# Kernel optimization log

Hardware: AMD Instinct MI355X
Metric: run time of the kernel (lower is better)

Reference implementation:

```python
import jax, jax.numpy as jnp
import numpy as np

N_NODES = 100_000
N_EDGES = 3_200_000
F_IN = 64
HID = 16
N_CLASSES = 4


def setup_inputs() -> dict:
    key = jax.random.key(0)
    ks = jax.random.split(key, 9)
    x = jax.random.normal(ks[0], (N_NODES, F_IN), dtype=jnp.float32)
    edge_index = jax.random.randint(ks[1], (2, N_EDGES), 0, N_NODES, dtype=jnp.int64)
    edge_weight = jax.random.uniform(ks[2], (N_EDGES,), dtype=jnp.float32)
    # Glorot-style init for the three GCN layer weights, zero bias (PyG default)
    W1 = jax.random.normal(ks[3], (F_IN, HID), dtype=jnp.float32) * (1.0 / np.sqrt(F_IN))
    b1 = jnp.zeros((HID,), jnp.float32)
    W3 = jax.random.normal(ks[4], (HID, HID), dtype=jnp.float32) * (1.0 / np.sqrt(HID))
    b3 = jnp.zeros((HID,), jnp.float32)
    W2 = jax.random.normal(ks[5], (HID, N_CLASSES), dtype=jnp.float32) * (1.0 / np.sqrt(HID))
    b2 = jnp.zeros((N_CLASSES,), jnp.float32)
    return {"x": x, "edge_index": edge_index, "edge_weight": edge_weight,
            "W1": W1, "b1": b1, "W3": W3, "b3": b3, "W2": W2, "b2": b2}


def reference(x, edge_index, edge_weight, W1, b1, W3, b3, W2, b2):
    n = x.shape[0]
    # GCNConv default: add self-loops with weight 1, symmetric deg^-1/2 norm
    loop = jnp.arange(n, dtype=edge_index.dtype)
    row = jnp.concatenate([edge_index[0], loop])  # source nodes
    col = jnp.concatenate([edge_index[1], loop])  # target nodes
    ew = jnp.concatenate([edge_weight, jnp.ones((n,), edge_weight.dtype)])
    deg = jax.ops.segment_sum(ew, col, num_segments=n)
    dinv = jnp.where(deg > 0, jax.lax.rsqrt(deg), 0.0)
    norm = dinv[row] * ew * dinv[col]  # [E+N]

    def gcn_conv(h, W, b):
        h = h @ W                                  # [N, out] small matmul first
        msg = norm[:, None] * h[row]               # gather + scale, [E+N, out]
        return jax.ops.segment_sum(msg, col, num_segments=n) + b

    h = jax.nn.relu(gcn_conv(x, W1, b1))
    # dropout is identity in eval mode (training=False)
    h = jax.nn.relu(gcn_conv(h, W3, b3))
    h = gcn_conv(h, W2, b2)
    return jax.nn.log_softmax(h, axis=1)
```

## Files before the change

kernel.cpp:

```cpp
#include <hip/hip_runtime.h>
#include <math.h>

#define NN 100000
#define NE 3200000
#define F_IN 64
#define HID 16
#define NC 4

#define SZB 256
#define NB 391
#define CAP 10240
#define CH 8192
#define NCH 391

typedef _Float16 half_t;
typedef _Float16 h4f __attribute__((ext_vector_type(4)));

__global__ __launch_bounds__(512) void k_initcur(int* __restrict__ cursor) {
    int i = threadIdx.x;
    if (i < NB) cursor[i] = i * CAP;
}

__global__ __launch_bounds__(1024) void k_bin(const int* __restrict__ row,
                                              const int* __restrict__ col,
                                              const float* __restrict__ ew,
                                              int* __restrict__ cursor,
                                              uint2* __restrict__ bin) {
    __shared__ int h[NB];
    __shared__ int lstart[NB + 1];
    __shared__ int gbase[NB];
    __shared__ int ps[512];
    __shared__ uint2 stage[CH];
    int tid = threadIdx.x;
    for (int i = tid; i < NB; i += 1024) h[i] = 0;
    __syncthreads();
    int e0 = blockIdx.x * CH;
    int e1 = min(e0 + CH, NE);
    int eCnt = e1 - e0;
    for (int i = e0 + tid * 4; i < e1; i += 1024 * 4) {
        int4 c4 = *(const int4*)(col + i);
        atomicAdd(&h[c4.x >> 8], 1);
        atomicAdd(&h[c4.y >> 8], 1);
        atomicAdd(&h[c4.z >> 8], 1);
        atomicAdd(&h[c4.w >> 8], 1);
    }
    __syncthreads();
    int c0 = (tid < NB) ? h[tid] : 0;
    if (tid < 512) ps[tid] = c0;
    for (int off = 1; off < 512; off <<= 1) {
        __syncthreads();
        int v = (tid < 512 && tid >= off) ? ps[tid - off] : 0;
        __syncthreads();
        if (tid < 512) ps[tid] += v;
    }
    __syncthreads();
    if (tid < NB) {
        int ex = ps[tid] - c0;
        lstart[tid] = ex;
        h[tid] = ex;
        if (c0) gbase[tid] = atomicAdd(&cursor[tid], c0);
    }
    if (tid == 0) lstart[NB] = eCnt;
    __syncthreads();
    for (int i = e0 + tid * 4; i < e1; i += 1024 * 4) {
        int4 c4 = *(const int4*)(col + i);
        int4 r4 = *(const int4*)(row + i);
        float4 w4 = *(const float4*)(ew + i);
        int p;
        p = atomicAdd(&h[c4.x >> 8], 1);
        stage[p] = make_uint2(((unsigned)r4.x << 8) | (c4.x & 255), __float_as_uint(w4.x));
        p = atomicAdd(&h[c4.y >> 8], 1);
        stage[p] = make_uint2(((unsigned)r4.y << 8) | (c4.y & 255), __float_as_uint(w4.y));
        p = atomicAdd(&h[c4.z >> 8], 1);
        stage[p] = make_uint2(((unsigned)r4.z << 8) | (c4.z & 255), __float_as_uint(w4.z));
        p = atomicAdd(&h[c4.w >> 8], 1);
        stage[p] = make_uint2(((unsigned)r4.w << 8) | (c4.w & 255), __float_as_uint(w4.w));
    }
    __syncthreads();
    for (int i = tid; i < eCnt; i += 1024) {
        int lo = 0, hi = NB;
        while (hi - lo > 1) {
            int mid = (lo + hi) >> 1;
            if (lstart[mid] <= i) lo = mid; else hi = mid;
        }
        int d = gbase[lo] + (i - lstart[lo]);
        if (d < (lo + 1) * CAP)
            bin[d] = stage[i];
    }
}

__global__ __launch_bounds__(1024) void k_sort(const uint2* __restrict__ bin,
                                               const int* __restrict__ cursor,
                                               unsigned* __restrict__ ekey,
                                               half_t* __restrict__ ew16,
                                               int2* __restrict__ nodeptr2,
                                               float* __restrict__ dinv) {
    __shared__ int cnt[SZB];
    __shared__ float wdeg[SZB];
    __shared__ int ps[SZB];
    __shared__ int curp[SZB];
    __shared__ int mpad_s;
    __shared__ unsigned skey_st[CAP];
    __shared__ half_t sw_st[CAP];
    int b = blockIdx.x, tid = threadIdx.x;
    if (tid < SZB) { cnt[tid] = 0; wdeg[tid] = 0.0f; }
    __syncthreads();
    int s = b * CAP;
    int e = min(cursor[b], s + CAP);
    for (int i = s + tid; i < e; i += 1024) {
        uint2 u = bin[i];
        int cl = u.x & 255;
        atomicAdd(&cnt[cl], 1);
        atomicAdd(&wdeg[cl], __uint_as_float(u.y));
    }
    __syncthreads();
    int pc = (tid < SZB) ? ((cnt[tid] + 3) & ~3) : 0;
    if (tid < SZB) ps[tid] = pc;
    for (int off = 1; off < SZB; off <<= 1) {
        __syncthreads();
        int v = (tid < SZB && tid >= off) ? ps[tid - off] : 0;
        __syncthreads();
        if (tid < SZB) ps[tid] += v;
    }
    __syncthreads();
    if (tid < SZB) {
        int ex = ps[tid] - pc;
        curp[tid] = ex;
        int n = b * SZB + tid;
        if (n < NN) {
            nodeptr2[n] = make_int2(s + ex, s + ex + pc);
            dinv[n] = rsqrtf(1.0f + wdeg[tid]);
        }
        if (tid == SZB - 1) mpad_s = ps[tid];
    }
    __syncthreads();
    int mpad = mpad_s;
    for (int i = tid; i < mpad; i += 1024) {
        skey_st[i] = 0u;
        sw_st[i] = (half_t)0.0f;
    }
    __syncthreads();
    for (int i = s + tid; i < e; i += 1024) {
        uint2 u = bin[i];
        int cl = u.x & 255;
        int pos = atomicAdd(&curp[cl], 1);
        skey_st[pos] = u.x >> 8;
        sw_st[pos] = (half_t)__uint_as_float(u.y);
    }
    __syncthreads();
    for (int i = tid; i < mpad; i += 1024) {
        ekey[s + i] = skey_st[i];
        ew16[s + i] = sw_st[i];
    }
}

__global__ __launch_bounds__(256) void k_xform1(const float* __restrict__ x,
                                                const float* __restrict__ W,
                                                const float* __restrict__ dinv,
                                                half_t* __restrict__ tt) {
    __shared__ float Ws[F_IN * HID];
    for (int i = threadIdx.x; i < F_IN * HID; i += 256) Ws[i] = W[i];
    __syncthreads();
    int n = blockIdx.x * blockDim.x + threadIdx.x;
    if (n >= NN) return;
    float acc[HID];
#pragma unroll
    for (int j = 0; j < HID; j++) acc[j] = 0.0f;
    const float4* xp = (const float4*)(x + (size_t)n * F_IN);
#pragma unroll
    for (int k4 = 0; k4 < F_IN / 4; k4++) {
        float4 v = xp[k4];
        int k = k4 * 4;
#pragma unroll
        for (int j = 0; j < HID; j++) {
            acc[j] += v.x * Ws[(k + 0) * HID + j];
            acc[j] += v.y * Ws[(k + 1) * HID + j];
            acc[j] += v.z * Ws[(k + 2) * HID + j];
            acc[j] += v.w * Ws[(k + 3) * HID + j];
        }
    }
    float di = dinv[n];
    h4f* op = (h4f*)(tt + (size_t)n * HID);
#pragma unroll
    for (int g = 0; g < 4; g++) {
        h4f o;
        o.x = (half_t)(di * acc[g * 4 + 0]);
        o.y = (half_t)(di * acc[g * 4 + 1]);
        o.z = (half_t)(di * acc[g * 4 + 2]);
        o.w = (half_t)(di * acc[g * 4 + 3]);
        op[g] = o;
    }
}

template <int DN>
__global__ __launch_bounds__(256) void k_aggf(const unsigned* __restrict__ ekey,
                                              const half_t* __restrict__ ew16,
                                              const int2* __restrict__ nptr,
                                              const half_t* __restrict__ tt_in,
                                              const float* __restrict__ bias,
                                              const float* __restrict__ dinv,
                                              const float* __restrict__ Wn,
                                              half_t* __restrict__ tt_out) {
    __shared__ float Ws[HID * DN];
    if (threadIdx.x < HID * DN) Ws[threadIdx.x] = Wn[threadIdx.x];
    __syncthreads();
    int tid = blockIdx.x * 256 + threadIdx.x;
    int n = tid >> 2;
    int l = tid & 3;
    if (n >= NN) return;
    int2 p = nptr[n];
    const h4f* ttp = (const h4f*)tt_in;
    h4f sv = ttp[n * 4 + l];
    float ax = 0.f, ay = 0.f, az = 0.f, aw = 0.f;
    for (int base = p.x; base < p.y; base += 4) {
        int4 k4 = *(const int4*)(ekey + base);
        h4f w4 = *(const h4f*)(ew16 + base);
        h4f v0 = ttp[k4.x * 4 + l];
        h4f v1 = ttp[k4.y * 4 + l];
        h4f v2 = ttp[k4.z * 4 + l];
        h4f v3 = ttp[k4.w * 4 + l];
        float w0 = (float)w4.x, w1 = (float)w4.y, w2 = (float)w4.z, w3 = (float)w4.w;
        ax += w0 * (float)v0.x; ay += w0 * (float)v0.y; az += w0 * (float)v0.z; aw += w0 * (float)v0.w;
        ax += w1 * (float)v1.x; ay += w1 * (float)v1.y; az += w1 * (float)v1.z; aw += w1 * (float)v1.w;
        ax += w2 * (float)v2.x; ay += w2 * (float)v2.y; az += w2 * (float)v2.z; aw += w2 * (float)v2.w;
        ax += w3 * (float)v3.x; ay += w3 * (float)v3.y; az += w3 * (float)v3.z; aw += w3 * (float)v3.w;
    }
    float di = dinv[n];
    const float4* b4p = (const float4*)bias;
    float4 b4 = b4p[l];
    float hreg[4];
    hreg[0] = fmaxf(b4.x + di * (ax + (float)sv.x), 0.f);
    hreg[1] = fmaxf(b4.y + di * (ay + (float)sv.y), 0.f);
    hreg[2] = fmaxf(b4.z + di * (az + (float)sv.z), 0.f);
    hreg[3] = fmaxf(b4.w + di * (aw + (float)sv.w), 0.f);
    if (DN == 16) {
        float ox = 0.f, oy = 0.f, oz = 0.f, ow = 0.f;
#pragma unroll
        for (int k = 0; k < HID; k++) {
            float hk = __shfl(hreg[k & 3], k >> 2, 4);
            const float4 wk = *(const float4*)&Ws[k * 16 + 4 * l];
            ox += hk * wk.x; oy += hk * wk.y; oz += hk * wk.z; ow += hk * wk.w;
        }
        h4f ov;
        ov.x = (half_t)(di * ox); ov.y = (half_t)(di * oy);
        ov.z = (half_t)(di * oz); ov.w = (half_t)(di * ow);
        ((h4f*)tt_out)[n * 4 + l] = ov;
    } else {
        float o = 0.f;
#pragma unroll
        for (int k = 0; k < HID; k++) {
            float hk = __shfl(hreg[k & 3], k >> 2, 4);
            o += hk * Ws[k * DN + l];
        }
        tt_out[(size_t)n * DN + l] = (half_t)(di * o);
    }
}

__global__ __launch_bounds__(256) void k_agg4sm(const unsigned* __restrict__ ekey,
                                                const half_t* __restrict__ ew16,
                                                const int2* __restrict__ nptr,
                                                const half_t* __restrict__ tt,
                                                const float* __restrict__ bias,
                                                const float* __restrict__ dinv,
                                                float* __restrict__ out) {
    int tid = blockIdx.x * 256 + threadIdx.x;
    int n = tid >> 2;
    int l = tid & 3;
    if (n >= NN) return;
    int2 p = nptr[n];
    float self = (float)tt[n * 4 + l];
    float acc = 0.f;
    for (int base = p.x; base < p.y; base += 4) {
        int4 k4 = *(const int4*)(ekey + base);
        h4f w4 = *(const h4f*)(ew16 + base);
        acc += (float)w4.x * (float)tt[k4.x * 4 + l];
        acc += (float)w4.y * (float)tt[k4.y * 4 + l];
        acc += (float)w4.z * (float)tt[k4.z * 4 + l];
        acc += (float)w4.w * (float)tt[k4.w * 4 + l];
    }
    float di = dinv[n];
    float logit = bias[l] + di * (acc + self);
    float m = logit;
    m = fmaxf(m, __shfl_xor(m, 1, 4));
    m = fmaxf(m, __shfl_xor(m, 2, 4));
    float ex = expf(logit - m);
    float s = ex;
    s += __shfl_xor(s, 1, 4);
    s += __shfl_xor(s, 2, 4);
    out[n * 4 + l] = logit - m - logf(s);
}

extern "C" void kernel_launch(void* const* d_in, const int* in_sizes, int n_in,
                              void* d_out, int out_size, void* d_ws, size_t ws_size,
                              hipStream_t stream) {
    const float* x  = (const float*)d_in[0];
    const int*   ei = (const int*)d_in[1];
    const float* ew = (const float*)d_in[2];
    const float* W1 = (const float*)d_in[3];
    const float* b1 = (const float*)d_in[4];
    const float* W3 = (const float*)d_in[5];
    const float* b3 = (const float*)d_in[6];
    const float* W2 = (const float*)d_in[7];
    const float* b2 = (const float*)d_in[8];
    float* out = (float*)d_out;

    const int* row = ei;
    const int* col = ei + NE;

    const size_t NEP = (size_t)NB * CAP;
    char* ws = (char*)d_ws;
    size_t off = 0;
    float*    dinv     = (float*)(ws + off);    off += 400000;
    int2*     nodeptr2 = (int2*)(ws + off);     off += 800000;
    int*      cursor   = (int*)(ws + off);      off += 2048;
    unsigned* ekey     = (unsigned*)(ws + off); off += NEP * 4;
    half_t*   ew16     = (half_t*)(ws + off);   off += NEP * 2;
    uint2*    bin      = (uint2*)(ws + off);    off += NEP * 8;
    half_t*   tt1      = (half_t*)(ws + off);   off += (size_t)NN * HID * 2;
    half_t*   tt2      = (half_t*)(ws + off);   off += (size_t)NN * HID * 2;
    half_t*   tt3      = (half_t*)(ws + off);   off += (size_t)NN * NC * 2;

    k_initcur<<<1, 512, 0, stream>>>(cursor);
    k_bin<<<NCH, 1024, 0, stream>>>(row, col, ew, cursor, bin);
    k_sort<<<NB, 1024, 0, stream>>>(bin, cursor, ekey, ew16, nodeptr2, dinv);

    int gN = (NN + 255) / 256;
    int gA = (NN * 4 + 255) / 256;

    k_xform1<<<gN, 256, 0, stream>>>(x, W1, dinv, tt1);
    k_aggf<HID><<<gA, 256, 0, stream>>>(ekey, ew16, nodeptr2, tt1, b1, dinv, W3, tt2);
    k_aggf<NC><<<gA, 256, 0, stream>>>(ekey, ew16, nodeptr2, tt2, b3, dinv, W2, tt3);
    k_agg4sm<<<gA, 256, 0, stream>>>(ekey, ew16, nodeptr2, tt3, b2, dinv, out);
}
```

Baseline: 255.1 us.

## Pack edge key and fp16 weight into one word; fuse first transform into sort

New measurement: 249.9 us. 1.02x faster.

```diff
diff --git a/kernel.cpp b/kernel.cpp
--- a/kernel.cpp
+++ b/kernel.cpp
@@ -16,9 +16,11 @@
 typedef _Float16 half_t;
 typedef _Float16 h4f __attribute__((ext_vector_type(4)));
 
-__global__ __launch_bounds__(512) void k_initcur(int* __restrict__ cursor) {
-    int i = threadIdx.x;
-    if (i < NB) cursor[i] = i * CAP;
+__device__ __forceinline__ float upw(int pk) {
+    unsigned short us = (unsigned short)(pk & 0x7fff);
+    half_t h;
+    __builtin_memcpy(&h, &us, 2);
+    return (float)h;
 }
 
 __global__ __launch_bounds__(1024) void k_bin(const int* __restrict__ row,
@@ -58,7 +60,7 @@
         int ex = ps[tid] - c0;
         lstart[tid] = ex;
         h[tid] = ex;
-        if (c0) gbase[tid] = atomicAdd(&cursor[tid], c0);
+        if (c0) gbase[tid] = tid * CAP + atomicAdd(&cursor[tid], c0);
     }
     if (tid == 0) lstart[NB] = eCnt;
     __syncthreads();
@@ -91,22 +93,26 @@
 
 __global__ __launch_bounds__(1024) void k_sort(const uint2* __restrict__ bin,
                                                const int* __restrict__ cursor,
-                                               unsigned* __restrict__ ekey,
-                                               half_t* __restrict__ ew16,
+                                               const float* __restrict__ x,
+                                               const float* __restrict__ W1,
+                                               unsigned* __restrict__ epk,
                                                int2* __restrict__ nodeptr2,
-                                               float* __restrict__ dinv) {
+                                               float* __restrict__ dinv,
+                                               half_t* __restrict__ tt1) {
     __shared__ int cnt[SZB];
     __shared__ float wdeg[SZB];
     __shared__ int ps[SZB];
     __shared__ int curp[SZB];
     __shared__ int mpad_s;
-    __shared__ unsigned skey_st[CAP];
-    __shared__ half_t sw_st[CAP];
+    __shared__ unsigned stage[CAP];
+    __shared__ float Ws[F_IN * HID];
     int b = blockIdx.x, tid = threadIdx.x;
     if (tid < SZB) { cnt[tid] = 0; wdeg[tid] = 0.0f; }
+    for (int i = tid; i < F_IN * HID; i += 1024) Ws[i] = W1[i];
     __syncthreads();
     int s = b * CAP;
-    int e = min(cursor[b], s + CAP);
+    int m = min(cursor[b], CAP);
+    int e = s + m;
     for (int i = s + tid; i < e; i += 1024) {
         uint2 u = bin[i];
         int cl = u.x & 255;
@@ -135,66 +141,56 @@
     }
     __syncthreads();
     int mpad = mpad_s;
-    for (int i = tid; i < mpad; i += 1024) {
-        skey_st[i] = 0u;
-        sw_st[i] = (half_t)0.0f;
-    }
+    for (int i = tid; i < mpad; i += 1024) stage[i] = 0u;
     __syncthreads();
     for (int i = s + tid; i < e; i += 1024) {
         uint2 u = bin[i];
         int cl = u.x & 255;
         int pos = atomicAdd(&curp[cl], 1);
-        skey_st[pos] = u.x >> 8;
-        sw_st[pos] = (half_t)__uint_as_float(u.y);
-    }
-    __syncthreads();
-    for (int i = tid; i < mpad; i += 1024) {
-        ekey[s + i] = skey_st[i];
-        ew16[s + i] = sw_st[i];
-    }
-}
-
-__global__ __launch_bounds__(256) void k_xform1(const float* __restrict__ x,
-                                                const float* __restrict__ W,
-                                                const float* __restrict__ dinv,
-                                                half_t* __restrict__ tt) {
-    __shared__ float Ws[F_IN * HID];
-    for (int i = threadIdx.x; i < F_IN * HID; i += 256) Ws[i] = W[i];
-    __syncthreads();
-    int n = blockIdx.x * blockDim.x + threadIdx.x;
-    if (n >= NN) return;
-    float acc[HID];
-#pragma unroll
-    for (int j = 0; j < HID; j++) acc[j] = 0.0f;
-    const float4* xp = (const float4*)(x + (size_t)n * F_IN);
-#pragma unroll
-    for (int k4 = 0; k4 < F_IN / 4; k4++) {
-        float4 v = xp[k4];
-        int k = k4 * 4;
+        half_t hw = (half_t)__uint_as_float(u.y);
+        unsigned short hb;
+        __builtin_memcpy(&hb, &hw, 2);
+        stage[pos] = ((u.x >> 8) << 15) | (unsigned)(hb & 0x7fff);
+    }
+    __syncthreads();
+    for (int i = tid; i < mpad; i += 1024) epk[s + i] = stage[i];
+
+    int nl = tid >> 2, l = tid & 3;
+    int n = b * SZB + nl;
+    if (n < NN) {
+        float part[HID];
+#pragma unroll
+        for (int j = 0; j < HID; j++) part[j] = 0.0f;
+        const float4* xp = (const float4*)(x + (size_t)n * F_IN) + l * 4;
+#pragma unroll
+        for (int k4 = 0; k4 < 4; k4++) {
+            float4 v = xp[k4];
+            int k = l * 16 + k4 * 4;
+#pragma unroll
+            for (int j = 0; j < HID; j++) {
+                part[j] += v.x * Ws[(k + 0) * HID + j];
+                part[j] += v.y * Ws[(k + 1) * HID + j];
+                part[j] += v.z * Ws[(k + 2) * HID + j];
+                part[j] += v.w * Ws[(k + 3) * HID + j];
+            }
+        }
 #pragma unroll
         for (int j = 0; j < HID; j++) {
-            acc[j] += v.x * Ws[(k + 0) * HID + j];
-            acc[j] += v.y * Ws[(k + 1) * HID + j];
-            acc[j] += v.z * Ws[(k + 2) * HID + j];
-            acc[j] += v.w * Ws[(k + 3) * HID + j];
-        }
-    }
-    float di = dinv[n];
-    h4f* op = (h4f*)(tt + (size_t)n * HID);
-#pragma unroll
-    for (int g = 0; g < 4; g++) {
+            part[j] += __shfl_xor(part[j], 1, 4);
+            part[j] += __shfl_xor(part[j], 2, 4);
+        }
+        float di = rsqrtf(1.0f + wdeg[nl]);
         h4f o;
-        o.x = (half_t)(di * acc[g * 4 + 0]);
-        o.y = (half_t)(di * acc[g * 4 + 1]);
-        o.z = (half_t)(di * acc[g * 4 + 2]);
-        o.w = (half_t)(di * acc[g * 4 + 3]);
-        op[g] = o;
+        o.x = (half_t)(di * part[4 * l + 0]);
+        o.y = (half_t)(di * part[4 * l + 1]);
+        o.z = (half_t)(di * part[4 * l + 2]);
+        o.w = (half_t)(di * part[4 * l + 3]);
+        ((h4f*)tt1)[n * 4 + l] = o;
     }
 }
 
 template <int DN>
-__global__ __launch_bounds__(256) void k_aggf(const unsigned* __restrict__ ekey,
-                                              const half_t* __restrict__ ew16,
+__global__ __launch_bounds__(256) void k_aggf(const unsigned* __restrict__ epk,
                                               const int2* __restrict__ nptr,
                                               const half_t* __restrict__ tt_in,
                                               const float* __restrict__ bias,
@@ -213,13 +209,16 @@
     h4f sv = ttp[n * 4 + l];
     float ax = 0.f, ay = 0.f, az = 0.f, aw = 0.f;
     for (int base = p.x; base < p.y; base += 4) {
-        int4 k4 = *(const int4*)(ekey + base);
-        h4f w4 = *(const h4f*)(ew16 + base);
-        h4f v0 = ttp[k4.x * 4 + l];
-        h4f v1 = ttp[k4.y * 4 + l];
-        h4f v2 = ttp[k4.z * 4 + l];
-        h4f v3 = ttp[k4.w * 4 + l];
-        float w0 = (float)w4.x, w1 = (float)w4.y, w2 = (float)w4.z, w3 = (float)w4.w;
+        int4 q = *(const int4*)(epk + base);
+        int r0 = ((unsigned)q.x) >> 15;
+        int r1 = ((unsigned)q.y) >> 15;
+        int r2 = ((unsigned)q.z) >> 15;
+        int r3 = ((unsigned)q.w) >> 15;
+        float w0 = upw(q.x), w1 = upw(q.y), w2 = upw(q.z), w3 = upw(q.w);
+        h4f v0 = ttp[r0 * 4 + l];
+        h4f v1 = ttp[r1 * 4 + l];
+        h4f v2 = ttp[r2 * 4 + l];
+        h4f v3 = ttp[r3 * 4 + l];
         ax += w0 * (float)v0.x; ay += w0 * (float)v0.y; az += w0 * (float)v0.z; aw += w0 * (float)v0.w;
         ax += w1 * (float)v1.x; ay += w1 * (float)v1.y; az += w1 * (float)v1.z; aw += w1 * (float)v1.w;
         ax += w2 * (float)v2.x; ay += w2 * (float)v2.y; az += w2 * (float)v2.z; aw += w2 * (float)v2.w;
@@ -256,8 +255,7 @@
     }
 }
 
-__global__ __launch_bounds__(256) void k_agg4sm(const unsigned* __restrict__ ekey,
-                                                const half_t* __restrict__ ew16,
+__global__ __launch_bounds__(256) void k_agg4sm(const unsigned* __restrict__ epk,
                                                 const int2* __restrict__ nptr,
                                                 const half_t* __restrict__ tt,
                                                 const float* __restrict__ bias,
@@ -271,12 +269,15 @@
     float self = (float)tt[n * 4 + l];
     float acc = 0.f;
     for (int base = p.x; base < p.y; base += 4) {
-        int4 k4 = *(const int4*)(ekey + base);
-        h4f w4 = *(const h4f*)(ew16 + base);
-        acc += (float)w4.x * (float)tt[k4.x * 4 + l];
-        acc += (float)w4.y * (float)tt[k4.y * 4 + l];
-        acc += (float)w4.z * (float)tt[k4.z * 4 + l];
-        acc += (float)w4.w * (float)tt[k4.w * 4 + l];
+        int4 q = *(const int4*)(epk + base);
+        int r0 = ((unsigned)q.x) >> 15;
+        int r1 = ((unsigned)q.y) >> 15;
+        int r2 = ((unsigned)q.z) >> 15;
+        int r3 = ((unsigned)q.w) >> 15;
+        acc += upw(q.x) * (float)tt[r0 * 4 + l];
+        acc += upw(q.y) * (float)tt[r1 * 4 + l];
+        acc += upw(q.z) * (float)tt[r2 * 4 + l];
+        acc += upw(q.w) * (float)tt[r3 * 4 + l];
     }
     float di = dinv[n];
     float logit = bias[l] + di * (acc + self);
@@ -313,22 +314,20 @@
     float*    dinv     = (float*)(ws + off);    off += 400000;
     int2*     nodeptr2 = (int2*)(ws + off);     off += 800000;
     int*      cursor   = (int*)(ws + off);      off += 2048;
-    unsigned* ekey     = (unsigned*)(ws + off); off += NEP * 4;
-    half_t*   ew16     = (half_t*)(ws + off);   off += NEP * 2;
+    unsigned* epk      = (unsigned*)(ws + off); off += NEP * 4;
     uint2*    bin      = (uint2*)(ws + off);    off += NEP * 8;
     half_t*   tt1      = (half_t*)(ws + off);   off += (size_t)NN * HID * 2;
     half_t*   tt2      = (half_t*)(ws + off);   off += (size_t)NN * HID * 2;
     half_t*   tt3      = (half_t*)(ws + off);   off += (size_t)NN * NC * 2;
 
-    k_initcur<<<1, 512, 0, stream>>>(cursor);
+    hipMemsetAsync(cursor, 0, NB * sizeof(int), stream);
+
     k_bin<<<NCH, 1024, 0, stream>>>(row, col, ew, cursor, bin);
-    k_sort<<<NB, 1024, 0, stream>>>(bin, cursor, ekey, ew16, nodeptr2, dinv);
-
-    int gN = (NN + 255) / 256;
+    k_sort<<<NB, 1024, 0, stream>>>(bin, cursor, x, W1, epk, nodeptr2, dinv, tt1);
+
     int gA = (NN * 4 + 255) / 256;
 
-    k_xform1<<<gN, 256, 0, stream>>>(x, W1, dinv, tt1);
-    k_aggf<HID><<<gA, 256, 0, stream>>>(ekey, ew16, nodeptr2, tt1, b1, dinv, W3, tt2);
-    k_aggf<NC><<<gA, 256, 0, stream>>>(ekey, ew16, nodeptr2, tt2, b3, dinv, W2, tt3);
-    k_agg4sm<<<gA, 256, 0, stream>>>(ekey, ew16, nodeptr2, tt3, b2, dinv, out);
-}
+    k_aggf<HID><<<gA, 256, 0, stream>>>(epk, nodeptr2, tt1, b1, dinv, W3, tt2);
+    k_aggf<NC><<<gA, 256, 0, stream>>>(epk, nodeptr2, tt2, b3, dinv, W2, tt3);
+    k_agg4sm<<<gA, 256, 0, stream>>>(epk, nodeptr2, tt3, b2, dinv, out);
+}
```
